# Performance work log

Measured on AMD Instinct MI355X. Metric: run time of the kernel, lower is better.

## Reference

```python
import jax, jax.numpy as jnp
import numpy as np

B, C, H, W = 4, 512, 64, 64
CQ = C // 4  # query/key channels


def setup_inputs() -> dict:
    key = jax.random.key(0)
    ks = jax.random.split(key, 8)
    s_in = 1.0 / np.sqrt(C)
    return {
        "x": jax.random.normal(ks[0], (B, C, H, W), dtype=jnp.float32),
        "Wf_w": jax.random.normal(ks[1], (CQ, C), dtype=jnp.float32) * s_in,
        "Wf_b": jax.random.normal(ks[2], (CQ,), dtype=jnp.float32) * 0.01,
        "Wh_w": jax.random.normal(ks[3], (CQ, C), dtype=jnp.float32) * s_in,
        "Wh_b": jax.random.normal(ks[4], (CQ,), dtype=jnp.float32) * 0.01,
        "Wl_w": jax.random.normal(ks[5], (C, C), dtype=jnp.float32) * s_in,
        "Wl_b": jax.random.normal(ks[6], (C,), dtype=jnp.float32) * 0.01,
        "alpha": jax.random.uniform(ks[7], (1,), dtype=jnp.float32),
    }


def reference(x, Wf_w, Wf_b, Wh_w, Wh_b, Wl_w, Wl_b, alpha):
    b, c, h, w = x.shape
    n = h * w
    xr = x.reshape(b, c, n)  # (B, C, N)
    # 1x1 convs == per-pixel linear projections
    f = jnp.einsum('oc,bcn->bon', Wf_w, xr) + Wf_b[None, :, None]  # (B, C/4, N)
    k = jnp.einsum('oc,bcn->bon', Wh_w, xr) + Wh_b[None, :, None]  # (B, C/4, N)
    v = jnp.einsum('oc,bcn->bon', Wl_w, xr) + Wl_b[None, :, None]  # (B, C,   N)
    # t[b, i, j] = <f[:, i], k[:, j]>  -> (B, N, N)
    scores = jnp.einsum('boi,boj->bij', f, k)
    att = jax.nn.softmax(scores, axis=-1)
    # out[b, c, i] = sum_j v[b, c, j] * att[b, i, j]  (bmm with att^T)
    out = jnp.einsum('bcj,bij->bci', v, att)
    out = out.reshape(b, c, h, w)
    return out * alpha[0] + x
```

## Files before the change

### kernel.cpp

```cpp
#include <hip/hip_runtime.h>
#include <hip/hip_bf16.h>

typedef _Float16 f16;
typedef _Float16 f16x4 __attribute__((ext_vector_type(4)));
typedef _Float16 f16x8 __attribute__((ext_vector_type(8)));
typedef float f32x4 __attribute__((ext_vector_type(4)));

constexpr int BATCH = 4, C = 512, CQ = 128, N = 4096;
constexpr int OALL = 768;

constexpr size_t WS_FT   = 0;
constexpr size_t WS_KT   = WS_FT   + (size_t)BATCH * N * CQ * 2;
constexpr size_t WS_V    = WS_KT   + (size_t)BATCH * N * CQ * 2;
constexpr size_t WS_WALL = WS_V    + (size_t)BATCH * C * N * 2;
constexpr size_t WS_BALL = WS_WALL + (size_t)OALL * C * 2;

__global__ void prep_weights(const float* __restrict__ Wf_w, const float* __restrict__ Wf_b,
                             const float* __restrict__ Wh_w, const float* __restrict__ Wh_b,
                             const float* __restrict__ Wl_w, const float* __restrict__ Wl_b,
                             f16* __restrict__ wall, float* __restrict__ ball) {
    int i = blockIdx.x * 256 + threadIdx.x;
    if (i < OALL * C) {
        int o = i >> 9, c = i & 511;
        float v = (o < 128) ? Wf_w[o * C + c]
                : (o < 256) ? Wh_w[(o - 128) * C + c]
                            : Wl_w[(o - 256) * C + c];
        wall[i] = (f16)v;
    }
    if (i < OALL)
        ball[i] = (i < 128) ? Wf_b[i] : (i < 256) ? Wh_b[i - 128] : Wl_b[i - 256];
}

__global__ void __launch_bounds__(512) proj_all(const float* __restrict__ x, const f16* __restrict__ wall,
                                                const float* __restrict__ ball,
                                                f16* __restrict__ ft, f16* __restrict__ kt,
                                                f16* __restrict__ v) {
    __shared__ __align__(16) f16 xl[64][72];
    const int tid = threadIdx.x;
    const int wv  = tid >> 6;
    const int lane = tid & 63;
    const int li = lane & 15, lg = lane >> 4;
    const int b  = blockIdx.x >> 6;
    const int n0 = (blockIdx.x & 63) * 64;
    const int ob = wv * 96;
    const int nn = tid & 63, cg = tid >> 6;

    f32x4 acc[6][4] = {};
    for (int ch = 0; ch < 8; ++ch) {
        __syncthreads();
        {
            const float* xs = x + ((size_t)(b * C) + ch * 64 + cg * 8) * N + n0 + nn;
#pragma unroll
            for (int r = 0; r < 8; ++r)
                xl[nn][cg * 8 + r] = (f16)xs[(size_t)r * N];
        }
        __syncthreads();
#pragma unroll
        for (int ks = 0; ks < 2; ++ks) {
            f16x8 xfr[4];
#pragma unroll
            for (int nf = 0; nf < 4; ++nf)
                xfr[nf] = *(const f16x8*)(&xl[nf * 16 + li][ks * 32 + lg * 8]);
#pragma unroll
            for (int of = 0; of < 6; ++of) {
                f16x8 wfr = *(const f16x8*)(wall + (size_t)(ob + of * 16 + li) * C + ch * 64 + ks * 32 + lg * 8);
#pragma unroll
                for (int nf = 0; nf < 4; ++nf)
                    acc[of][nf] = __builtin_amdgcn_mfma_f32_16x16x32_f16(xfr[nf], wfr, acc[of][nf], 0, 0, 0);
            }
        }
    }
#pragma unroll
    for (int of = 0; of < 6; ++of) {
        const int o = ob + of * 16 + li;
        const float bias = ball[o];
#pragma unroll
        for (int nf = 0; nf < 4; ++nf)
#pragma unroll
            for (int r = 0; r < 4; ++r) {
                const int n = n0 + nf * 16 + lg * 4 + r;
                const f16 val = (f16)(acc[of][nf][r] + bias);
                if (o < 128) {
                    ft[(size_t)(b * N + n) * CQ + o] = val;
                } else if (o < 256) {
                    const int ck = o - 128;
                    kt[((size_t)b * N + n) * 128 + ck] = val;
                } else {
                    const int c = o - 256;
                    v[(((size_t)b * 32 + (c >> 4)) * 512 + (n >> 3)) * 128 + (c & 15) * 8 + (n & 7)] = val;
                }
            }
    }
}

__global__ void __launch_bounds__(512, 2) attn(const f16* __restrict__ ft, const f16* __restrict__ kt,
                                               const f16* __restrict__ v,
                                               const float* __restrict__ x, const float* __restrict__ alphap,
                                               float* __restrict__ out) {
    __shared__ __align__(16) f16 pbuf[64 * 128];
    __shared__ float smax[8][4][16];
    __shared__ float ssum[8][4][16];

    const int tid  = threadIdx.x;
    const int wv   = tid >> 6;
    const int lane = tid & 63;
    const int li = lane & 15, lg = lane >> 4;
    const int swl = li & 7;
    const int v0 = blockIdx.x;
    const int b  = (v0 & 7) >> 1;
    const int it = ((v0 & 1) << 5) | (v0 >> 3);
    const int i0 = it * 64;
    const int c0 = wv * 64;

    f16x8 fb[4][4];
#pragma unroll
    for (int f = 0; f < 4; ++f) {
        const f16* fp = ft + (size_t)(b * N + i0 + f * 16 + li) * CQ + lg * 8;
#pragma unroll
        for (int ks = 0; ks < 4; ++ks) fb[f][ks] = *(const f16x8*)(fp + ks * 32);
    }

    const f16* kL = kt + ((size_t)b * N + wv * 16 + li) * 128 + lg * 8;
    f16x8 kf[4];
#pragma unroll
    for (int ks = 0; ks < 4; ++ks) kf[ks] = *(const f16x8*)(kL + ks * 32);

    const f16* vb2 = v + (((size_t)b * 32 + wv * 4) * 512 + lg) * 128 + li * 8;
    f32x4 oacc[4][4] = {};
    float ms[4] = {-1e30f, -1e30f, -1e30f, -1e30f};
    float ls[4] = {0.f, 0.f, 0.f, 0.f};

    for (int t = 0; t < 32; ++t) {
        const size_t jb0 = (size_t)t * 16;
        f16x8 kfn[4];
        const size_t knext = (size_t)((t < 31) ? (t + 1) : 0) * 128 * 128;
#pragma unroll
        for (int ks = 0; ks < 4; ++ks) kfn[ks] = *(const f16x8*)(kL + knext + ks * 32);

        f32x4 s[4] = {};
        __builtin_amdgcn_s_setprio(1);
#pragma unroll
        for (int ks = 0; ks < 4; ++ks)
#pragma unroll
            for (int f = 0; f < 4; ++f)
                s[f] = __builtin_amdgcn_mfma_f32_16x16x32_f16(kf[ks], fb[f][ks], s[f], 0, 0, 0);
        __builtin_amdgcn_s_setprio(0);

        float tm[4];
#pragma unroll
        for (int f = 0; f < 4; ++f) {
            float t0 = fmaxf(fmaxf(s[f][0], s[f][1]), fmaxf(s[f][2], s[f][3]));
            t0 = fmaxf(t0, __shfl_xor(t0, 16));
            t0 = fmaxf(t0, __shfl_xor(t0, 32));
            tm[f] = t0;
        }
        if (lane < 16) {
#pragma unroll
            for (int f = 0; f < 4; ++f) smax[wv][f][li] = tm[f];
        }
        f16x8 va[2][4];
#pragma unroll
        for (int cf = 0; cf < 4; ++cf) va[0][cf] = *(const f16x8*)(vb2 + ((size_t)cf * 512 + jb0) * 128);
        __syncthreads();
        float gm[4];
#pragma unroll
        for (int f = 0; f < 4; ++f) {
            float m0 = smax[0][f][li];
#pragma unroll
            for (int w = 1; w < 8; ++w) m0 = fmaxf(m0, smax[w][f][li]);
            gm[f] = m0;
        }
#pragma unroll
        for (int cf = 0; cf < 4; ++cf) va[1][cf] = *(const f16x8*)(vb2 + ((size_t)cf * 512 + jb0 + 4) * 128);
#pragma unroll
        for (int f = 0; f < 4; ++f) {
            if (!__all(gm[f] <= ms[f] + 8.0f)) {
                float mn = fmaxf(ms[f], gm[f]), sc = __expf(ms[f] - mn);
                ms[f] = mn; ls[f] *= sc;
#pragma unroll
                for (int cf = 0; cf < 4; ++cf) oacc[cf][f] *= sc;
            }
        }
        const int jl = wv * 16 + lg * 4;
        const int gg = (jl >> 3) ^ swl;
        float ps[4];
#pragma unroll
        for (int f = 0; f < 4; ++f) {
            f16x4 pk;
            float p0 = 0.f;
#pragma unroll
            for (int r = 0; r < 4; ++r) { float p = __expf(s[f][r] - ms[f]); p0 += p; pk[r] = (f16)p; }
            *(f16x4*)(&pbuf[(f * 16 + li) * 128 + gg * 8 + (jl & 7)]) = pk;
            ps[f] = p0;
        }
#pragma unroll
        for (int f = 0; f < 4; ++f) {
            ps[f] += __shfl_xor(ps[f], 16);
            ps[f] += __shfl_xor(ps[f], 32);
        }
        if (lane < 16) {
#pragma unroll
            for (int f = 0; f < 4; ++f) ssum[wv][f][li] = ps[f];
        }
        __syncthreads();
#pragma unroll
        for (int f = 0; f < 4; ++f) {
            float a0 = 0.f;
#pragma unroll
            for (int w = 0; w < 8; ++w) a0 += ssum[w][f][li];
            ls[f] += a0;
        }
#pragma unroll
        for (int kf2 = 0; kf2 < 4; ++kf2) {
            const int cur = kf2 & 1;
            const int g = (kf2 * 4 + lg) ^ swl;
            f16x8 pb[4];
#pragma unroll
            for (int f = 0; f < 4; ++f)
                pb[f] = *(const f16x8*)(&pbuf[(f * 16 + li) * 128 + g * 8]);
            f16x8 vv0 = va[cur][0], vv1 = va[cur][1], vv2 = va[cur][2], vv3 = va[cur][3];
            if (kf2 < 2) {
#pragma unroll
                for (int cf = 0; cf < 4; ++cf)
                    va[cur][cf] = *(const f16x8*)(vb2 + ((size_t)cf * 512 + jb0 + (kf2 + 2) * 4) * 128);
            }
            __builtin_amdgcn_s_setprio(1);
#pragma unroll
            for (int f = 0; f < 4; ++f) {
                oacc[0][f] = __builtin_amdgcn_mfma_f32_16x16x32_f16(vv0, pb[f], oacc[0][f], 0, 0, 0);
                oacc[1][f] = __builtin_amdgcn_mfma_f32_16x16x32_f16(vv1, pb[f], oacc[1][f], 0, 0, 0);
                oacc[2][f] = __builtin_amdgcn_mfma_f32_16x16x32_f16(vv2, pb[f], oacc[2][f], 0, 0, 0);
                oacc[3][f] = __builtin_amdgcn_mfma_f32_16x16x32_f16(vv3, pb[f], oacc[3][f], 0, 0, 0);
            }
            __builtin_amdgcn_s_setprio(0);
        }
#pragma unroll
        for (int ks = 0; ks < 4; ++ks) kf[ks] = kfn[ks];
    }

    const float alpha = alphap[0];
#pragma unroll
    for (int f = 0; f < 4; ++f) {
        const float invf = alpha / ls[f];
        const float* xp = x + (size_t)(b * C + c0) * N + i0 + f * 16 + li;
        float* op = out + (size_t)(b * C + c0) * N + i0 + f * 16 + li;
#pragma unroll
        for (int cf = 0; cf < 4; ++cf)
#pragma unroll
            for (int r = 0; r < 4; ++r) {
                const int cl = cf * 16 + lg * 4 + r;
                op[(size_t)cl * N] = oacc[cf][f][r] * invf + xp[(size_t)cl * N];
            }
    }
}

extern "C" void kernel_launch(void* const* d_in, const int* in_sizes, int n_in,
                              void* d_out, int out_size, void* d_ws, size_t ws_size,
                              hipStream_t stream) {
    const float* x     = (const float*)d_in[0];
    const float* Wf_w  = (const float*)d_in[1];
    const float* Wf_b  = (const float*)d_in[2];
    const float* Wh_w  = (const float*)d_in[3];
    const float* Wh_b  = (const float*)d_in[4];
    const float* Wl_w  = (const float*)d_in[5];
    const float* Wl_b  = (const float*)d_in[6];
    const float* alpha = (const float*)d_in[7];
    char* ws = (char*)d_ws;
    f16*   ftb  = (f16*)(ws + WS_FT);
    f16*   ktb  = (f16*)(ws + WS_KT);
    f16*   vb   = (f16*)(ws + WS_V);
    f16*   wall = (f16*)(ws + WS_WALL);
    float* ball = (float*)(ws + WS_BALL);
    float* out  = (float*)d_out;

    prep_weights<<<dim3((OALL * C + 255) / 256), dim3(256), 0, stream>>>(Wf_w, Wf_b, Wh_w, Wh_b, Wl_w, Wl_b, wall, ball);
    proj_all<<<dim3(256), dim3(512), 0, stream>>>(x, wall, ball, ftb, ktb, vb);
    attn<<<dim3(256), dim3(512), 0, stream>>>(ftb, ktb, vb, x, alpha, out);
}
```

Baseline: 160.5 us.

## Double-buffer projection x tiles and software-pipeline score computation in attention loop

The projection kernel now double-buffers the x tile in shared memory, loading the next channel chunk into registers while MFMAs run on the current one, so only one barrier per chunk is needed. The attention kernel is software-pipelined: the QK^T scores and row max for the next key tile are computed at the end of the current iteration, and the V fragment loads are moved later, ahead of the second barrier. The goal is to overlap global loads with MFMA work and shorten the critical path between barriers. In exchange it uses more shared memory and registers, and the attention loop still has an extra barrier per iteration, so occupancy could drop.

```diff
diff --git a/kernel.cpp b/kernel.cpp
--- a/kernel.cpp
+++ b/kernel.cpp
@@ -35,7 +35,7 @@
                                                 const float* __restrict__ ball,
                                                 f16* __restrict__ ft, f16* __restrict__ kt,
                                                 f16* __restrict__ v) {
-    __shared__ __align__(16) f16 xl[64][72];
+    __shared__ __align__(16) f16 xl[2][64][72];
     const int tid = threadIdx.x;
     const int wv  = tid >> 6;
     const int lane = tid & 63;
@@ -45,22 +45,29 @@
     const int ob = wv * 96;
     const int nn = tid & 63, cg = tid >> 6;
 
+    {
+        const float* xs = x + ((size_t)(b * C) + cg * 8) * N + n0 + nn;
+#pragma unroll
+        for (int r = 0; r < 8; ++r)
+            xl[0][nn][cg * 8 + r] = (f16)xs[(size_t)r * N];
+    }
+    __syncthreads();
+
     f32x4 acc[6][4] = {};
     for (int ch = 0; ch < 8; ++ch) {
-        __syncthreads();
-        {
-            const float* xs = x + ((size_t)(b * C) + ch * 64 + cg * 8) * N + n0 + nn;
-#pragma unroll
-            for (int r = 0; r < 8; ++r)
-                xl[nn][cg * 8 + r] = (f16)xs[(size_t)r * N];
-        }
-        __syncthreads();
+        const int cur = ch & 1;
+        float xr[8];
+        if (ch < 7) {
+            const float* xs = x + ((size_t)(b * C) + (ch + 1) * 64 + cg * 8) * N + n0 + nn;
+#pragma unroll
+            for (int r = 0; r < 8; ++r) xr[r] = xs[(size_t)r * N];
+        }
 #pragma unroll
         for (int ks = 0; ks < 2; ++ks) {
             f16x8 xfr[4];
 #pragma unroll
             for (int nf = 0; nf < 4; ++nf)
-                xfr[nf] = *(const f16x8*)(&xl[nf * 16 + li][ks * 32 + lg * 8]);
+                xfr[nf] = *(const f16x8*)(&xl[cur][nf * 16 + li][ks * 32 + lg * 8]);
 #pragma unroll
             for (int of = 0; of < 6; ++of) {
                 f16x8 wfr = *(const f16x8*)(wall + (size_t)(ob + of * 16 + li) * C + ch * 64 + ks * 32 + lg * 8);
@@ -69,6 +76,11 @@
                     acc[of][nf] = __builtin_amdgcn_mfma_f32_16x16x32_f16(xfr[nf], wfr, acc[of][nf], 0, 0, 0);
             }
         }
+        if (ch < 7) {
+#pragma unroll
+            for (int r = 0; r < 8; ++r) xl[cur ^ 1][nn][cg * 8 + r] = (f16)xr[r];
+        }
+        __syncthreads();
     }
 #pragma unroll
     for (int of = 0; of < 6; ++of) {
@@ -121,14 +133,33 @@
     }
 
     const f16* kL = kt + ((size_t)b * N + wv * 16 + li) * 128 + lg * 8;
-    f16x8 kf[4];
-#pragma unroll
-    for (int ks = 0; ks < 4; ++ks) kf[ks] = *(const f16x8*)(kL + ks * 32);
-
     const f16* vb2 = v + (((size_t)b * 32 + wv * 4) * 512 + lg) * 128 + li * 8;
+
     f32x4 oacc[4][4] = {};
     float ms[4] = {-1e30f, -1e30f, -1e30f, -1e30f};
     float ls[4] = {0.f, 0.f, 0.f, 0.f};
+
+    f32x4 s[4] = {};
+    {
+        f16x8 kf[4];
+#pragma unroll
+        for (int ks = 0; ks < 4; ++ks) kf[ks] = *(const f16x8*)(kL + ks * 32);
+        __builtin_amdgcn_s_setprio(1);
+#pragma unroll
+        for (int ks = 0; ks < 4; ++ks)
+#pragma unroll
+            for (int f = 0; f < 4; ++f)
+                s[f] = __builtin_amdgcn_mfma_f32_16x16x32_f16(kf[ks], fb[f][ks], s[f], 0, 0, 0);
+        __builtin_amdgcn_s_setprio(0);
+#pragma unroll
+        for (int f = 0; f < 4; ++f) {
+            float t0 = fmaxf(fmaxf(s[f][0], s[f][1]), fmaxf(s[f][2], s[f][3]));
+            t0 = fmaxf(t0, __shfl_xor(t0, 16));
+            t0 = fmaxf(t0, __shfl_xor(t0, 32));
+            if (lane < 16) smax[wv][f][li] = t0;
+        }
+    }
+    __syncthreads();
 
     for (int t = 0; t < 32; ++t) {
         const size_t jb0 = (size_t)t * 16;
@@ -137,31 +168,6 @@
 #pragma unroll
         for (int ks = 0; ks < 4; ++ks) kfn[ks] = *(const f16x8*)(kL + knext + ks * 32);
 
-        f32x4 s[4] = {};
-        __builtin_amdgcn_s_setprio(1);
-#pragma unroll
-        for (int ks = 0; ks < 4; ++ks)
-#pragma unroll
-            for (int f = 0; f < 4; ++f)
-                s[f] = __builtin_amdgcn_mfma_f32_16x16x32_f16(kf[ks], fb[f][ks], s[f], 0, 0, 0);
-        __builtin_amdgcn_s_setprio(0);
-
-        float tm[4];
-#pragma unroll
-        for (int f = 0; f < 4; ++f) {
-            float t0 = fmaxf(fmaxf(s[f][0], s[f][1]), fmaxf(s[f][2], s[f][3]));
-            t0 = fmaxf(t0, __shfl_xor(t0, 16));
-            t0 = fmaxf(t0, __shfl_xor(t0, 32));
-            tm[f] = t0;
-        }
-        if (lane < 16) {
-#pragma unroll
-            for (int f = 0; f < 4; ++f) smax[wv][f][li] = tm[f];
-        }
-        f16x8 va[2][4];
-#pragma unroll
-        for (int cf = 0; cf < 4; ++cf) va[0][cf] = *(const f16x8*)(vb2 + ((size_t)cf * 512 + jb0) * 128);
-        __syncthreads();
         float gm[4];
 #pragma unroll
         for (int f = 0; f < 4; ++f) {
@@ -170,8 +176,6 @@
             for (int w = 1; w < 8; ++w) m0 = fmaxf(m0, smax[w][f][li]);
             gm[f] = m0;
         }
-#pragma unroll
-        for (int cf = 0; cf < 4; ++cf) va[1][cf] = *(const f16x8*)(vb2 + ((size_t)cf * 512 + jb0 + 4) * 128);
 #pragma unroll
         for (int f = 0; f < 4; ++f) {
             if (!__all(gm[f] <= ms[f] + 8.0f)) {
@@ -202,6 +206,11 @@
 #pragma unroll
             for (int f = 0; f < 4; ++f) ssum[wv][f][li] = ps[f];
         }
+        f16x8 va[2][4];
+#pragma unroll
+        for (int cf = 0; cf < 4; ++cf) va[0][cf] = *(const f16x8*)(vb2 + ((size_t)cf * 512 + jb0) * 128);
+#pragma unroll
+        for (int cf = 0; cf < 4; ++cf) va[1][cf] = *(const f16x8*)(vb2 + ((size_t)cf * 512 + jb0 + 4) * 128);
         __syncthreads();
 #pragma unroll
         for (int f = 0; f < 4; ++f) {
@@ -234,8 +243,25 @@
             }
             __builtin_amdgcn_s_setprio(0);
         }
-#pragma unroll
-        for (int ks = 0; ks < 4; ++ks) kf[ks] = kfn[ks];
+        if (t < 31) {
+#pragma unroll
+            for (int f = 0; f < 4; ++f) s[f] = (f32x4){0.f, 0.f, 0.f, 0.f};
+            __builtin_amdgcn_s_setprio(1);
+#pragma unroll
+            for (int ks = 0; ks < 4; ++ks)
+#pragma unroll
+                for (int f = 0; f < 4; ++f)
+                    s[f] = __builtin_amdgcn_mfma_f32_16x16x32_f16(kfn[ks], fb[f][ks], s[f], 0, 0, 0);
+            __builtin_amdgcn_s_setprio(0);
+#pragma unroll
+            for (int f = 0; f < 4; ++f) {
+                float t0 = fmaxf(fmaxf(s[f][0], s[f][1]), fmaxf(s[f][2], s[f][3]));
+                t0 = fmaxf(t0, __shfl_xor(t0, 16));
+                t0 = fmaxf(t0, __shfl_xor(t0, 32));
+                if (lane < 16) smax[wv][f][li] = t0;
+            }
+            __syncthreads();
+        }
     }
 
     const float alpha = alphap[0];
```

New measurement: 193.9 us. +20.8%, slower.

## Double the key tile per iteration to halve softmax barriers

Applied to the files above, without the earlier changes.

Each iteration now processes 256 keys instead of 128: every wave computes two 16-key score slices, and the P buffer doubles to 64x256. The loop count halves, so the two __syncthreads and the cross-wave max and sum reductions run half as often per key. The K-fragment prefetch is restructured so the second slice loads while the first slice's MFMAs run. The cost is more registers (two score sets, two K fragment sets) and double the LDS, which may hurt occupancy under launch_bounds(512,2).

```diff
diff --git a/kernel.cpp b/kernel.cpp
--- a/kernel.cpp
+++ b/kernel.cpp
@@ -97,7 +97,7 @@
                                                const f16* __restrict__ v,
                                                const float* __restrict__ x, const float* __restrict__ alphap,
                                                float* __restrict__ out) {
-    __shared__ __align__(16) f16 pbuf[64 * 128];
+    __shared__ __align__(16) f16 pbuf[64 * 256];
     __shared__ float smax[8][4][16];
     __shared__ float ssum[8][4][16];
 
@@ -120,43 +120,50 @@
         for (int ks = 0; ks < 4; ++ks) fb[f][ks] = *(const f16x8*)(fp + ks * 32);
     }
 
-    const f16* kL = kt + ((size_t)b * N + wv * 16 + li) * 128 + lg * 8;
-    f16x8 kf[4];
-#pragma unroll
-    for (int ks = 0; ks < 4; ++ks) kf[ks] = *(const f16x8*)(kL + ks * 32);
+    const f16* kL = kt + ((size_t)b * N + wv * 32 + li) * 128 + lg * 8;
+    f16x8 kfA[4], kfB[4];
+#pragma unroll
+    for (int ks = 0; ks < 4; ++ks) kfA[ks] = *(const f16x8*)(kL + ks * 32);
 
     const f16* vb2 = v + (((size_t)b * 32 + wv * 4) * 512 + lg) * 128 + li * 8;
     f32x4 oacc[4][4] = {};
     float ms[4] = {-1e30f, -1e30f, -1e30f, -1e30f};
     float ls[4] = {0.f, 0.f, 0.f, 0.f};
 
-    for (int t = 0; t < 32; ++t) {
-        const size_t jb0 = (size_t)t * 16;
-        f16x8 kfn[4];
-        const size_t knext = (size_t)((t < 31) ? (t + 1) : 0) * 128 * 128;
-#pragma unroll
-        for (int ks = 0; ks < 4; ++ks) kfn[ks] = *(const f16x8*)(kL + knext + ks * 32);
-
-        f32x4 s[4] = {};
+    for (int t = 0; t < 16; ++t) {
+        const size_t jb0 = (size_t)t * 32;
+        const size_t ktile = (size_t)t * 256 * 128;
+#pragma unroll
+        for (int ks = 0; ks < 4; ++ks)
+            kfB[ks] = *(const f16x8*)(kL + ktile + (size_t)16 * 128 + ks * 32);
+        f32x4 s[2][4] = {};
         __builtin_amdgcn_s_setprio(1);
 #pragma unroll
         for (int ks = 0; ks < 4; ++ks)
 #pragma unroll
             for (int f = 0; f < 4; ++f)
-                s[f] = __builtin_amdgcn_mfma_f32_16x16x32_f16(kf[ks], fb[f][ks], s[f], 0, 0, 0);
+                s[0][f] = __builtin_amdgcn_mfma_f32_16x16x32_f16(kfA[ks], fb[f][ks], s[0][f], 0, 0, 0);
         __builtin_amdgcn_s_setprio(0);
-
-        float tm[4];
-#pragma unroll
-        for (int f = 0; f < 4; ++f) {
-            float t0 = fmaxf(fmaxf(s[f][0], s[f][1]), fmaxf(s[f][2], s[f][3]));
+        const size_t knext = (size_t)((t < 15) ? (t + 1) : 0) * 256 * 128;
+#pragma unroll
+        for (int ks = 0; ks < 4; ++ks)
+            kfA[ks] = *(const f16x8*)(kL + knext + ks * 32);
+        __builtin_amdgcn_s_setprio(1);
+#pragma unroll
+        for (int ks = 0; ks < 4; ++ks)
+#pragma unroll
+            for (int f = 0; f < 4; ++f)
+                s[1][f] = __builtin_amdgcn_mfma_f32_16x16x32_f16(kfB[ks], fb[f][ks], s[1][f], 0, 0, 0);
+        __builtin_amdgcn_s_setprio(0);
+
+#pragma unroll
+        for (int f = 0; f < 4; ++f) {
+            float t0 = fmaxf(fmaxf(s[0][f][0], s[0][f][1]), fmaxf(s[0][f][2], s[0][f][3]));
+            float t1 = fmaxf(fmaxf(s[1][f][0], s[1][f][1]), fmaxf(s[1][f][2], s[1][f][3]));
+            t0 = fmaxf(t0, t1);
             t0 = fmaxf(t0, __shfl_xor(t0, 16));
             t0 = fmaxf(t0, __shfl_xor(t0, 32));
-            tm[f] = t0;
-        }
-        if (lane < 16) {
-#pragma unroll
-            for (int f = 0; f < 4; ++f) smax[wv][f][li] = tm[f];
+            if (lane < 16) smax[wv][f][li] = t0;
         }
         f16x8 va[2][4];
 #pragma unroll
@@ -181,16 +188,19 @@
                 for (int cf = 0; cf < 4; ++cf) oacc[cf][f] *= sc;
             }
         }
-        const int jl = wv * 16 + lg * 4;
-        const int gg = (jl >> 3) ^ swl;
         float ps[4];
 #pragma unroll
         for (int f = 0; f < 4; ++f) {
-            f16x4 pk;
             float p0 = 0.f;
 #pragma unroll
-            for (int r = 0; r < 4; ++r) { float p = __expf(s[f][r] - ms[f]); p0 += p; pk[r] = (f16)p; }
-            *(f16x4*)(&pbuf[(f * 16 + li) * 128 + gg * 8 + (jl & 7)]) = pk;
+            for (int sl = 0; sl < 2; ++sl) {
+                const int jl = wv * 32 + sl * 16 + lg * 4;
+                const int gg = (jl >> 3) ^ swl;
+                f16x4 pk;
+#pragma unroll
+                for (int r = 0; r < 4; ++r) { float p = __expf(s[sl][f][r] - ms[f]); p0 += p; pk[r] = (f16)p; }
+                *(f16x4*)(&pbuf[(f * 16 + li) * 256 + gg * 8 + (jl & 7)]) = pk;
+            }
             ps[f] = p0;
         }
 #pragma unroll
@@ -211,18 +221,18 @@
             ls[f] += a0;
         }
 #pragma unroll
-        for (int kf2 = 0; kf2 < 4; ++kf2) {
-            const int cur = kf2 & 1;
-            const int g = (kf2 * 4 + lg) ^ swl;
+        for (int ph = 0; ph < 8; ++ph) {
+            const int cur = ph & 1;
+            const int g = (ph * 4 + lg) ^ swl;
             f16x8 pb[4];
 #pragma unroll
             for (int f = 0; f < 4; ++f)
-                pb[f] = *(const f16x8*)(&pbuf[(f * 16 + li) * 128 + g * 8]);
+                pb[f] = *(const f16x8*)(&pbuf[(f * 16 + li) * 256 + g * 8]);
             f16x8 vv0 = va[cur][0], vv1 = va[cur][1], vv2 = va[cur][2], vv3 = va[cur][3];
-            if (kf2 < 2) {
+            if (ph < 6) {
 #pragma unroll
                 for (int cf = 0; cf < 4; ++cf)
-                    va[cur][cf] = *(const f16x8*)(vb2 + ((size_t)cf * 512 + jb0 + (kf2 + 2) * 4) * 128);
+                    va[cur][cf] = *(const f16x8*)(vb2 + ((size_t)cf * 512 + jb0 + (ph + 2) * 4) * 128);
             }
             __builtin_amdgcn_s_setprio(1);
 #pragma unroll
@@ -234,8 +244,6 @@
             }
             __builtin_amdgcn_s_setprio(0);
         }
-#pragma unroll
-        for (int ks = 0; ks < 4; ++ks) kf[ks] = kfn[ks];
     }
 
     const float alpha = alphap[0];
```

After: 172.2 us. 1.07x slower.
